# Kernel optimization log

Measured on AMD Instinct MI355X. Metric: run time of the kernel, lower is better.

## Reference

```python
import jax, jax.numpy as jnp
import numpy as np

N_NODES = 100000
N_EDGES = 1600000
IN_C, HID_C, OUT_C = 128, 128, 64


def setup_inputs() -> dict:
    key = jax.random.key(0)
    ks = jax.random.split(key, 8)
    x = jax.random.normal(ks[0], (N_NODES, IN_C), dtype=jnp.float32)
    edge_index = jax.random.randint(ks[1], (2, N_EDGES), 0, N_NODES, dtype=jnp.int64)
    # SAGEConv params: lin_l (aggregated neighbors, with bias), lin_r (root, no bias)
    s1 = 1.0 / np.sqrt(IN_C)
    s2 = 1.0 / np.sqrt(HID_C)
    W1_l = jax.random.uniform(ks[2], (IN_C, HID_C), jnp.float32, -s1, s1)
    b1_l = jnp.zeros((HID_C,), jnp.float32)
    W1_r = jax.random.uniform(ks[3], (IN_C, HID_C), jnp.float32, -s1, s1)
    W2_l = jax.random.uniform(ks[4], (HID_C, OUT_C), jnp.float32, -s2, s2)
    b2_l = jnp.zeros((OUT_C,), jnp.float32)
    W2_r = jax.random.uniform(ks[5], (HID_C, OUT_C), jnp.float32, -s2, s2)
    return {"x": x, "edge_index": edge_index, "W1_l": W1_l, "b1_l": b1_l,
            "W1_r": W1_r, "W2_l": W2_l, "b2_l": b2_l, "W2_r": W2_r}


def _sage_conv(x, src, dst, W_l, b_l, W_r):
    # gather source features, scatter-max reduce onto destinations
    msg = x[src]                                             # [E, C]
    aggr = jax.ops.segment_max(msg, dst, num_segments=N_NODES)
    aggr = jnp.where(jnp.isfinite(aggr), aggr, 0.0)          # isolated nodes -> 0 (PyG behavior)
    return aggr @ W_l + b_l + x @ W_r


def reference(x, edge_index, W1_l, b1_l, W1_r, W2_l, b2_l, W2_r):
    src, dst = edge_index[0], edge_index[1]
    h = _sage_conv(x, src, dst, W1_l, b1_l, W1_r)
    h = jax.nn.relu(h)
    # dropout is identity in eval mode
    out = _sage_conv(h, src, dst, W2_l, b2_l, W2_r)
    return out
```

## Files before the change

kernel.cpp:

```cpp
#include <hip/hip_runtime.h>
#include <cstdint>

#define NNODES 100000
#define NEDGES 1600000
#define NBKT   196
#define CAP    9216
#define BIN_CHUNK 4096
#define GBIN ((NEDGES + BIN_CHUNK - 1) / BIN_CHUNK)
#define GCVT (NNODES * 16 / 256)
#define GWPK 24

typedef __attribute__((ext_vector_type(8))) __bf16 bf16x8;
typedef __attribute__((ext_vector_type(4))) float f32x4;
typedef short v2s __attribute__((ext_vector_type(2)));

__device__ __forceinline__ unsigned short f2bf_rne(float f) {
    unsigned int u = __float_as_uint(f);
    u += 0x7fffu + ((u >> 16) & 1u);
    return (unsigned short)(u >> 16);
}
__device__ __forceinline__ unsigned encdec(unsigned u) {
    return u ^ (((u & 0x80008000u) >> 15) * 0x7FFFu);
}
__device__ __forceinline__ unsigned pkmax(unsigned a, unsigned b) {
    v2s r = __builtin_elementwise_max(__builtin_bit_cast(v2s, a), __builtin_bit_cast(v2s, b));
    return __builtin_bit_cast(unsigned, r);
}
__device__ __forceinline__ uint4 pkmax4(uint4 a, uint4 b) {
    uint4 r;
    r.x = pkmax(a.x, b.x); r.y = pkmax(a.y, b.y);
    r.z = pkmax(a.z, b.z); r.w = pkmax(a.w, b.w);
    return r;
}


__global__ __launch_bounds__(256) void prep_kernel(
        const int* __restrict__ src, const int* __restrict__ dst,
        unsigned int* __restrict__ binArr, int* __restrict__ bucketFill,
        const float4* __restrict__ xin, uint4* __restrict__ xeout,
        const float* __restrict__ W1l, const float* __restrict__ W1r,
        const float* __restrict__ W2l, const float* __restrict__ W2r,
        uint4* __restrict__ Wf1, uint4* __restrict__ Wf2, int nE) {
    if (blockIdx.x >= GBIN + GCVT) {
        int t = (blockIdx.x - GBIN - GCVT) * 256 + threadIdx.x;
        unsigned short s[8];
        if (t < 4096) {
            int h = t >> 11, kt = (t >> 9) & 3, nt = (t >> 6) & 7, lane = t & 63;
            const float* W = h ? W1r : W1l;
            int k0 = kt * 32 + (lane >> 4) * 8;
            int col = nt * 16 + (lane & 15);
#pragma unroll
            for (int jj = 0; jj < 8; ++jj) s[jj] = f2bf_rne(W[(k0 + jj) * 128 + col]);
            uint4 o;
            o.x = (unsigned)s[0] | ((unsigned)s[1] << 16);
            o.y = (unsigned)s[2] | ((unsigned)s[3] << 16);
            o.z = (unsigned)s[4] | ((unsigned)s[5] << 16);
            o.w = (unsigned)s[6] | ((unsigned)s[7] << 16);
            Wf1[t] = o;
        } else {
            int u = t - 4096;
            int h = u >> 10, kt = (u >> 8) & 3, nt = (u >> 6) & 3, lane = u & 63;
            const float* W = h ? W2r : W2l;
            int k0 = kt * 32 + (lane >> 4) * 8;
            int col = nt * 16 + (lane & 15);
#pragma unroll
            for (int jj = 0; jj < 8; ++jj) s[jj] = f2bf_rne(W[(k0 + jj) * 64 + col]);
            uint4 o;
            o.x = (unsigned)s[0] | ((unsigned)s[1] << 16);
            o.y = (unsigned)s[2] | ((unsigned)s[3] << 16);
            o.z = (unsigned)s[4] | ((unsigned)s[5] << 16);
            o.w = (unsigned)s[6] | ((unsigned)s[7] << 16);
            Wf2[u] = o;
        }
        return;
    }
    if (blockIdx.x >= GBIN) {
        int t = (blockIdx.x - GBIN) * 256 + threadIdx.x;
        int s = t / (NNODES * 8);
        int rem = t - s * (NNODES * 8);
        int n = rem >> 3, j = rem & 7;
        int f = n * 32 + s * 16 + j * 2;
        float4 v0 = xin[f], v1 = xin[f + 1];
        uint4 o;
        o.x = encdec((unsigned)f2bf_rne(v0.x) | ((unsigned)f2bf_rne(v0.y) << 16));
        o.y = encdec((unsigned)f2bf_rne(v0.z) | ((unsigned)f2bf_rne(v0.w) << 16));
        o.z = encdec((unsigned)f2bf_rne(v1.x) | ((unsigned)f2bf_rne(v1.y) << 16));
        o.w = encdec((unsigned)f2bf_rne(v1.z) | ((unsigned)f2bf_rne(v1.w) << 16));
        xeout[t] = o;
        return;
    }
    __shared__ unsigned int stage[BIN_CHUNK];
    __shared__ unsigned char bof[BIN_CHUNK];
    __shared__ int cnt[256], cstart[256], cfill[256], gbase[256];
    const int tid = threadIdx.x;
    const int blockStart = blockIdx.x * BIN_CHUNK;
    const int chunkN = min(BIN_CHUNK, nE - blockStart);
    cnt[tid] = 0;
    __syncthreads();
    int myd[16], mys[16];
#pragma unroll
    for (int i = 0; i < 16; ++i) {
        int idx = i * 256 + tid;
        if (idx < chunkN) {
            myd[i] = dst[blockStart + idx];
            mys[i] = src[blockStart + idx];
            atomicAdd(&cnt[myd[i] >> 9], 1);
        }
    }
    __syncthreads();
    int v = cnt[tid];
    for (int off = 1; off < 256; off <<= 1) {
        int add = (tid >= off) ? cnt[tid - off] : 0;
        __syncthreads();
        cnt[tid] += add;
        __syncthreads();
    }
    cstart[tid] = cnt[tid] - v;
    cfill[tid] = cnt[tid] - v;
    if (tid < NBKT && v > 0) gbase[tid] = atomicAdd(&bucketFill[tid], v);
    __syncthreads();
#pragma unroll
    for (int i = 0; i < 16; ++i) {
        int idx = i * 256 + tid;
        if (idx < chunkN) {
            int b = myd[i] >> 9;
            int p = atomicAdd(&cfill[b], 1);
            stage[p] = ((unsigned)(myd[i] & 511) << 17) | (unsigned)mys[i];
            bof[p] = (unsigned char)b;
        }
    }
    __syncthreads();
#pragma unroll
    for (int i = 0; i < 16; ++i) {
        int idx = i * 256 + tid;
        if (idx < chunkN) {
            int b = bof[idx];
            int slot = gbase[b] + (idx - cstart[b]);
            if (slot < CAP) binArr[(size_t)b * CAP + slot] = stage[idx];
        }
    }
}

__global__ __launch_bounds__(512) void build_csr_kernel(
        const unsigned int* __restrict__ binArr, const int* __restrict__ bucketFill,
        unsigned int* __restrict__ sortedSrc,
        int* __restrict__ rowBeg, int* __restrict__ rowEnd) {
    __shared__ unsigned int stage[CAP];
    __shared__ int ncnt[512], nstart[512];
    const int b = blockIdx.x;
    const int t = threadIdx.x;
    const int cnt_b = min(bucketFill[b], CAP);
    ncnt[t] = 0;
    __syncthreads();
    for (int i = t; i < cnt_b; i += 512) {
        unsigned int e = binArr[(size_t)b * CAP + i];
        stage[i] = e;
        atomicAdd(&ncnt[e >> 17], 1);
    }
    __syncthreads();
    int v = ncnt[t];
    for (int off = 1; off < 512; off <<= 1) {
        int add = (t >= off) ? ncnt[t - off] : 0;
        __syncthreads();
        ncnt[t] += add;
        __syncthreads();
    }
    int start = ncnt[t] - v;
    nstart[t] = start;
    int n = (b << 9) + t;
    if (n < NNODES) {
        rowBeg[n] = b * CAP + start;
        rowEnd[n] = b * CAP + start + v;
    }
    __syncthreads();
    for (int i = t; i < cnt_b; i += 512) {
        unsigned int e = stage[i];
        int p = atomicAdd(&nstart[e >> 17], 1);
        sortedSrc[(size_t)b * CAP + p] = e & 0x1FFFFu;
    }
}

template<int BN, bool RELU, bool ENCOUT, typename OutT>
__global__ __launch_bounds__(256) void sage_fused(
        const uint4* __restrict__ xsl,
        const int* __restrict__ rowBeg,
        const int* __restrict__ rowEnd,
        const unsigned int* __restrict__ sortedSrc,
        const uint4* __restrict__ Wf,
        const float* __restrict__ bias,
        OutT* __restrict__ C,
        int nN) {
    constexpr int NT = BN / 16;
    constexpr int NTW = BN / 64;
    __shared__ uint4 lds[16][17];
    const int wv   = threadIdx.x >> 6;
    const int lane = threadIdx.x & 63;
    const int n0   = blockIdx.x * 16;

    {
        const int s  = wv & 1;
        const int nh = wv >> 1;
        const int k  = lane >> 3;
        const int j  = lane & 7;
        const int kb = k << 3;
        const int n  = n0 + nh * 8 + k;
        const size_t srow = (size_t)s * nN;

        const int beg = rowBeg[n], end = rowEnd[n];
        const int m = end - beg;

        int maxm = m;
        maxm = max(maxm, __shfl_xor(maxm, 8));
        maxm = max(maxm, __shfl_xor(maxm, 16));
        maxm = max(maxm, __shfl_xor(maxm, 32));

        int idv0 = 0, idv1 = 0;
        if (m > 0) {
            idv0 = (int)sortedSrc[min(beg + j,     end - 1)];
            idv1 = (int)sortedSrc[min(beg + 8 + j, end - 1)];
        }
        int a0 = __shfl(idv0, kb | 0), a1 = __shfl(idv0, kb | 1);
        int a2 = __shfl(idv0, kb | 2), a3 = __shfl(idv0, kb | 3);
        int a4 = __shfl(idv0, kb | 4), a5 = __shfl(idv0, kb | 5);
        int a6 = __shfl(idv0, kb | 6), a7 = __shfl(idv0, kb | 7);
        int b0 = __shfl(idv1, kb | 0), b1 = __shfl(idv1, kb | 1);
        int b2 = __shfl(idv1, kb | 2), b3 = __shfl(idv1, kb | 3);
        int b4 = __shfl(idv1, kb | 4), b5 = __shfl(idv1, kb | 5);
        int b6 = __shfl(idv1, kb | 6), b7 = __shfl(idv1, kb | 7);
        uint4 q0  = xsl[(srow + a0) * 8 + j];
        uint4 q1  = xsl[(srow + a1) * 8 + j];
        uint4 q2  = xsl[(srow + a2) * 8 + j];
        uint4 q3  = xsl[(srow + a3) * 8 + j];
        uint4 q4  = xsl[(srow + a4) * 8 + j];
        uint4 q5  = xsl[(srow + a5) * 8 + j];
        uint4 q6  = xsl[(srow + a6) * 8 + j];
        uint4 q7  = xsl[(srow + a7) * 8 + j];
        uint4 q8  = xsl[(srow + b0) * 8 + j];
        uint4 q9  = xsl[(srow + b1) * 8 + j];
        uint4 q10 = xsl[(srow + b2) * 8 + j];
        uint4 q11 = xsl[(srow + b3) * 8 + j];
        uint4 q12 = xsl[(srow + b4) * 8 + j];
        uint4 q13 = xsl[(srow + b5) * 8 + j];
        uint4 q14 = xsl[(srow + b6) * 8 + j];
        uint4 q15 = xsl[(srow + b7) * 8 + j];
        uint4 accA = pkmax4(pkmax4(pkmax4(q0, q1), pkmax4(q2, q3)),
                            pkmax4(pkmax4(q4, q5), pkmax4(q6, q7)));
        uint4 accB = pkmax4(pkmax4(pkmax4(q8, q9), pkmax4(q10, q11)),
                            pkmax4(pkmax4(q12, q13), pkmax4(q14, q15)));
        uint4 acc = pkmax4(accA, accB);

        for (int e0 = 16; e0 < maxm; e0 += 8) {
            if (e0 < m) {
                int idt = (int)sortedSrc[min(beg + e0 + j, end - 1)];
                int t0 = __shfl(idt, kb | 0), t1 = __shfl(idt, kb | 1);
                int t2 = __shfl(idt, kb | 2), t3 = __shfl(idt, kb | 3);
                int t4 = __shfl(idt, kb | 4), t5 = __shfl(idt, kb | 5);
                int t6 = __shfl(idt, kb | 6), t7 = __shfl(idt, kb | 7);
                uint4 u0 = xsl[(srow + t0) * 8 + j];
                uint4 u1 = xsl[(srow + t1) * 8 + j];
                uint4 u2 = xsl[(srow + t2) * 8 + j];
                uint4 u3 = xsl[(srow + t3) * 8 + j];
                uint4 u4 = xsl[(srow + t4) * 8 + j];
                uint4 u5 = xsl[(srow + t5) * 8 + j];
                uint4 u6 = xsl[(srow + t6) * 8 + j];
                uint4 u7 = xsl[(srow + t7) * 8 + j];
                acc = pkmax4(acc, pkmax4(pkmax4(pkmax4(u0, u1), pkmax4(u2, u3)),
                                         pkmax4(pkmax4(u4, u5), pkmax4(u6, u7))));
            }
        }

        uint4 o;
        if (m > 0) { o = acc; }
        else       { o.x = o.y = o.z = o.w = 0u; }
        lds[nh * 8 + k][s * 8 + j] = o;
    }
    __syncthreads();

    const int quad = lane >> 4;
    const int mrow = lane & 15;
    const int r    = n0 + mrow;

    f32x4 acc[NTW];
#pragma unroll
    for (int t = 0; t < NTW; ++t) acc[t] = (f32x4){0.f, 0.f, 0.f, 0.f};

#pragma unroll
    for (int kt = 0; kt < 4; ++kt) {
        const int q = kt * 4 + quad;
        uint4 ta = lds[mrow][q];
        uint4 tr = xsl[((size_t)(q >> 3) * nN + r) * 8 + (q & 7)];
        ta.x = encdec(ta.x); ta.y = encdec(ta.y); ta.z = encdec(ta.z); ta.w = encdec(ta.w);
        tr.x = encdec(tr.x); tr.y = encdec(tr.y); tr.z = encdec(tr.z); tr.w = encdec(tr.w);
        bf16x8 aa = __builtin_bit_cast(bf16x8, ta);
        bf16x8 ar = __builtin_bit_cast(bf16x8, tr);
#pragma unroll
        for (int t = 0; t < NTW; ++t) {
            const int ct = wv * NTW + t;
            bf16x8 wb0 = __builtin_bit_cast(bf16x8, Wf[(kt * NT + ct) * 64 + lane]);
            acc[t] = __builtin_amdgcn_mfma_f32_16x16x32_bf16(aa, wb0, acc[t], 0, 0, 0);
            bf16x8 wb1 = __builtin_bit_cast(bf16x8, Wf[((4 + kt) * NT + ct) * 64 + lane]);
            acc[t] = __builtin_amdgcn_mfma_f32_16x16x32_bf16(ar, wb1, acc[t], 0, 0, 0);
        }
    }

#pragma unroll
    for (int t = 0; t < NTW; ++t) {
        const int col = (wv * NTW + t) * 16 + mrow;
        const float bv = bias[col];
#pragma unroll
        for (int rr = 0; rr < 4; ++rr) {
            const int grow = n0 + quad * 4 + rr;
            float v = acc[t][rr] + bv;
            if (RELU) v = fmaxf(v, 0.0f);
            if constexpr (ENCOUT) {
                unsigned u = f2bf_rne(v);
                u ^= ((u >> 15) & 1u) * 0x7FFFu;
                C[((size_t)(col >> 6) * nN + grow) * 64 + (col & 63)] = (OutT)u;
            } else {
                C[(size_t)grow * BN + col] = (OutT)v;
            }
        }
    }
}

extern "C" void kernel_launch(void* const* d_in, const int* in_sizes, int n_in,
                              void* d_out, int out_size, void* d_ws, size_t ws_size,
                              hipStream_t stream) {
    const float* x   = (const float*)d_in[0];
    const int*   ei  = (const int*)d_in[1];
    const float* W1l = (const float*)d_in[2];
    const float* b1l = (const float*)d_in[3];
    const float* W1r = (const float*)d_in[4];
    const float* W2l = (const float*)d_in[5];
    const float* b2l = (const float*)d_in[6];
    const float* W2r = (const float*)d_in[7];
    float* out = (float*)d_out;

    const int* src = ei;
    const int* dst = ei + NEDGES;

    char* ws = (char*)d_ws;
    unsigned short* xe    = (unsigned short*)ws; ws += (size_t)NNODES * 128 * 2;
    unsigned short* he    = (unsigned short*)ws; ws += (size_t)NNODES * 128 * 2;
    unsigned int* binArr    = (unsigned int*)ws; ws += (size_t)NBKT * CAP * 4;
    unsigned int* sortedSrc = (unsigned int*)ws; ws += (size_t)NBKT * CAP * 4;
    int* rowBeg     = (int*)ws; ws += (size_t)NNODES * 4;
    int* rowEnd     = (int*)ws; ws += (size_t)NNODES * 4;
    int* bucketFill = (int*)ws; ws += 256 * 4;
    uint4* Wf1 = (uint4*)ws; ws += 4096 * 16;
    uint4* Wf2 = (uint4*)ws; ws += 2048 * 16;

    const int gFus = NNODES / 16;

    hipMemsetAsync(bucketFill, 0, 256 * sizeof(int), stream);
    prep_kernel<<<GBIN + GCVT + GWPK, 256, 0, stream>>>(
        src, dst, binArr, bucketFill, (const float4*)x, (uint4*)xe,
        W1l, W1r, W2l, W2r, Wf1, Wf2, NEDGES);
    build_csr_kernel<<<NBKT, 512, 0, stream>>>(binArr, bucketFill, sortedSrc, rowBeg, rowEnd);

    sage_fused<128, true, true, unsigned short><<<gFus, 256, 0, stream>>>(
        (const uint4*)xe, rowBeg, rowEnd, sortedSrc, Wf1, b1l, he, NNODES);
    sage_fused<64, false, false, float><<<gFus, 256, 0, stream>>>(
        (const uint4*)he, rowBeg, rowEnd, sortedSrc, Wf2, b2l, out, NNODES);
}
```

Measured before the change: 261.0 us.

## Process two node tiles per block, overlapping second gather with first GEMM

Each block now handles 32 nodes as two 16-node tiles with double-buffered shared memory. The second tile's first 16-neighbour gather is issued before the first tile's MFMA GEMM, so gather memory latency can hide behind matrix math. Grid size is halved. The cost is higher register pressure and fewer blocks, which may lower occupancy.

```diff
diff --git a/kernel.cpp b/kernel.cpp
--- a/kernel.cpp
+++ b/kernel.cpp
@@ -181,7 +181,7 @@
 }
 
 template<int BN, bool RELU, bool ENCOUT, typename OutT>
-__global__ __launch_bounds__(256) void sage_fused(
+__global__ __launch_bounds__(256) void sage_fused2(
         const uint4* __restrict__ xsl,
         const int* __restrict__ rowBeg,
         const int* __restrict__ rowEnd,
@@ -192,135 +192,176 @@
         int nN) {
     constexpr int NT = BN / 16;
     constexpr int NTW = BN / 64;
-    __shared__ uint4 lds[16][17];
+    __shared__ uint4 ldsb[2][16][17];
     const int wv   = threadIdx.x >> 6;
     const int lane = threadIdx.x & 63;
-    const int n0   = blockIdx.x * 16;
-
-    {
-        const int s  = wv & 1;
-        const int nh = wv >> 1;
-        const int k  = lane >> 3;
-        const int j  = lane & 7;
-        const int kb = k << 3;
-        const int n  = n0 + nh * 8 + k;
-        const size_t srow = (size_t)s * nN;
-
-        const int beg = rowBeg[n], end = rowEnd[n];
-        const int m = end - beg;
-
-        int maxm = m;
-        maxm = max(maxm, __shfl_xor(maxm, 8));
-        maxm = max(maxm, __shfl_xor(maxm, 16));
-        maxm = max(maxm, __shfl_xor(maxm, 32));
-
-        int idv0 = 0, idv1 = 0;
-        if (m > 0) {
-            idv0 = (int)sortedSrc[min(beg + j,     end - 1)];
-            idv1 = (int)sortedSrc[min(beg + 8 + j, end - 1)];
-        }
-        int a0 = __shfl(idv0, kb | 0), a1 = __shfl(idv0, kb | 1);
-        int a2 = __shfl(idv0, kb | 2), a3 = __shfl(idv0, kb | 3);
-        int a4 = __shfl(idv0, kb | 4), a5 = __shfl(idv0, kb | 5);
-        int a6 = __shfl(idv0, kb | 6), a7 = __shfl(idv0, kb | 7);
-        int b0 = __shfl(idv1, kb | 0), b1 = __shfl(idv1, kb | 1);
-        int b2 = __shfl(idv1, kb | 2), b3 = __shfl(idv1, kb | 3);
-        int b4 = __shfl(idv1, kb | 4), b5 = __shfl(idv1, kb | 5);
-        int b6 = __shfl(idv1, kb | 6), b7 = __shfl(idv1, kb | 7);
-        uint4 q0  = xsl[(srow + a0) * 8 + j];
-        uint4 q1  = xsl[(srow + a1) * 8 + j];
-        uint4 q2  = xsl[(srow + a2) * 8 + j];
-        uint4 q3  = xsl[(srow + a3) * 8 + j];
-        uint4 q4  = xsl[(srow + a4) * 8 + j];
-        uint4 q5  = xsl[(srow + a5) * 8 + j];
-        uint4 q6  = xsl[(srow + a6) * 8 + j];
-        uint4 q7  = xsl[(srow + a7) * 8 + j];
-        uint4 q8  = xsl[(srow + b0) * 8 + j];
-        uint4 q9  = xsl[(srow + b1) * 8 + j];
-        uint4 q10 = xsl[(srow + b2) * 8 + j];
-        uint4 q11 = xsl[(srow + b3) * 8 + j];
-        uint4 q12 = xsl[(srow + b4) * 8 + j];
-        uint4 q13 = xsl[(srow + b5) * 8 + j];
-        uint4 q14 = xsl[(srow + b6) * 8 + j];
-        uint4 q15 = xsl[(srow + b7) * 8 + j];
-        uint4 accA = pkmax4(pkmax4(pkmax4(q0, q1), pkmax4(q2, q3)),
-                            pkmax4(pkmax4(q4, q5), pkmax4(q6, q7)));
-        uint4 accB = pkmax4(pkmax4(pkmax4(q8, q9), pkmax4(q10, q11)),
-                            pkmax4(pkmax4(q12, q13), pkmax4(q14, q15)));
-        uint4 acc = pkmax4(accA, accB);
-
-        for (int e0 = 16; e0 < maxm; e0 += 8) {
-            if (e0 < m) {
-                int idt = (int)sortedSrc[min(beg + e0 + j, end - 1)];
-                int t0 = __shfl(idt, kb | 0), t1 = __shfl(idt, kb | 1);
-                int t2 = __shfl(idt, kb | 2), t3 = __shfl(idt, kb | 3);
-                int t4 = __shfl(idt, kb | 4), t5 = __shfl(idt, kb | 5);
-                int t6 = __shfl(idt, kb | 6), t7 = __shfl(idt, kb | 7);
-                uint4 u0 = xsl[(srow + t0) * 8 + j];
-                uint4 u1 = xsl[(srow + t1) * 8 + j];
-                uint4 u2 = xsl[(srow + t2) * 8 + j];
-                uint4 u3 = xsl[(srow + t3) * 8 + j];
-                uint4 u4 = xsl[(srow + t4) * 8 + j];
-                uint4 u5 = xsl[(srow + t5) * 8 + j];
-                uint4 u6 = xsl[(srow + t6) * 8 + j];
-                uint4 u7 = xsl[(srow + t7) * 8 + j];
-                acc = pkmax4(acc, pkmax4(pkmax4(pkmax4(u0, u1), pkmax4(u2, u3)),
-                                         pkmax4(pkmax4(u4, u5), pkmax4(u6, u7))));
-            }
-        }
-
-        uint4 o;
-        if (m > 0) { o = acc; }
-        else       { o.x = o.y = o.z = o.w = 0u; }
-        lds[nh * 8 + k][s * 8 + j] = o;
-    }
-    __syncthreads();
+    const int n0   = blockIdx.x * 32;
+
+    const int s  = wv & 1;
+    const int nh = wv >> 1;
+    const int k  = lane >> 3;
+    const int j  = lane & 7;
+    const int kb = k << 3;
+    const size_t srow = (size_t)s * nN;
+    const int nloc = nh * 8 + k;
 
     const int quad = lane >> 4;
     const int mrow = lane & 15;
-    const int r    = n0 + mrow;
-
-    f32x4 acc[NTW];
-#pragma unroll
-    for (int t = 0; t < NTW; ++t) acc[t] = (f32x4){0.f, 0.f, 0.f, 0.f};
-
-#pragma unroll
-    for (int kt = 0; kt < 4; ++kt) {
-        const int q = kt * 4 + quad;
-        uint4 ta = lds[mrow][q];
-        uint4 tr = xsl[((size_t)(q >> 3) * nN + r) * 8 + (q & 7)];
-        ta.x = encdec(ta.x); ta.y = encdec(ta.y); ta.z = encdec(ta.z); ta.w = encdec(ta.w);
-        tr.x = encdec(tr.x); tr.y = encdec(tr.y); tr.z = encdec(tr.z); tr.w = encdec(tr.w);
-        bf16x8 aa = __builtin_bit_cast(bf16x8, ta);
-        bf16x8 ar = __builtin_bit_cast(bf16x8, tr);
-#pragma unroll
-        for (int t = 0; t < NTW; ++t) {
-            const int ct = wv * NTW + t;
-            bf16x8 wb0 = __builtin_bit_cast(bf16x8, Wf[(kt * NT + ct) * 64 + lane]);
-            acc[t] = __builtin_amdgcn_mfma_f32_16x16x32_bf16(aa, wb0, acc[t], 0, 0, 0);
-            bf16x8 wb1 = __builtin_bit_cast(bf16x8, Wf[((4 + kt) * NT + ct) * 64 + lane]);
-            acc[t] = __builtin_amdgcn_mfma_f32_16x16x32_bf16(ar, wb1, acc[t], 0, 0, 0);
-        }
-    }
-
-#pragma unroll
-    for (int t = 0; t < NTW; ++t) {
-        const int col = (wv * NTW + t) * 16 + mrow;
-        const float bv = bias[col];
-#pragma unroll
-        for (int rr = 0; rr < 4; ++rr) {
-            const int grow = n0 + quad * 4 + rr;
-            float v = acc[t][rr] + bv;
-            if (RELU) v = fmaxf(v, 0.0f);
-            if constexpr (ENCOUT) {
-                unsigned u = f2bf_rne(v);
-                u ^= ((u >> 15) & 1u) * 0x7FFFu;
-                C[((size_t)(col >> 6) * nN + grow) * 64 + (col & 63)] = (OutT)u;
-            } else {
-                C[(size_t)grow * BN + col] = (OutT)v;
-            }
-        }
-    }
+
+    const int nT0 = n0 + nloc, nT1 = n0 + 16 + nloc;
+    const int beg0 = rowBeg[nT0], end0 = rowEnd[nT0];
+    const int beg1 = rowBeg[nT1], end1 = rowEnd[nT1];
+    const int m0 = end0 - beg0, m1 = end1 - beg1;
+    int p0a = 0, p0b = 0, p1a = 0, p1b = 0;
+    if (m0 > 0) {
+        p0a = (int)sortedSrc[min(beg0 + j,     end0 - 1)];
+        p0b = (int)sortedSrc[min(beg0 + 8 + j, end0 - 1)];
+    }
+    if (m1 > 0) {
+        p1a = (int)sortedSrc[min(beg1 + j,     end1 - 1)];
+        p1b = (int)sortedSrc[min(beg1 + 8 + j, end1 - 1)];
+    }
+
+#define GATHER16(idvA, idvB, accOut)                                           \
+    {                                                                          \
+        int a0 = __shfl(idvA, kb | 0), a1 = __shfl(idvA, kb | 1);              \
+        int a2 = __shfl(idvA, kb | 2), a3 = __shfl(idvA, kb | 3);              \
+        int a4 = __shfl(idvA, kb | 4), a5 = __shfl(idvA, kb | 5);              \
+        int a6 = __shfl(idvA, kb | 6), a7 = __shfl(idvA, kb | 7);              \
+        int b0 = __shfl(idvB, kb | 0), b1 = __shfl(idvB, kb | 1);              \
+        int b2 = __shfl(idvB, kb | 2), b3 = __shfl(idvB, kb | 3);              \
+        int b4 = __shfl(idvB, kb | 4), b5 = __shfl(idvB, kb | 5);              \
+        int b6 = __shfl(idvB, kb | 6), b7 = __shfl(idvB, kb | 7);              \
+        uint4 q0  = xsl[(srow + a0) * 8 + j];                                  \
+        uint4 q1  = xsl[(srow + a1) * 8 + j];                                  \
+        uint4 q2  = xsl[(srow + a2) * 8 + j];                                  \
+        uint4 q3  = xsl[(srow + a3) * 8 + j];                                  \
+        uint4 q4  = xsl[(srow + a4) * 8 + j];                                  \
+        uint4 q5  = xsl[(srow + a5) * 8 + j];                                  \
+        uint4 q6  = xsl[(srow + a6) * 8 + j];                                  \
+        uint4 q7  = xsl[(srow + a7) * 8 + j];                                  \
+        uint4 q8  = xsl[(srow + b0) * 8 + j];                                  \
+        uint4 q9  = xsl[(srow + b1) * 8 + j];                                  \
+        uint4 q10 = xsl[(srow + b2) * 8 + j];                                  \
+        uint4 q11 = xsl[(srow + b3) * 8 + j];                                  \
+        uint4 q12 = xsl[(srow + b4) * 8 + j];                                  \
+        uint4 q13 = xsl[(srow + b5) * 8 + j];                                  \
+        uint4 q14 = xsl[(srow + b6) * 8 + j];                                  \
+        uint4 q15 = xsl[(srow + b7) * 8 + j];                                  \
+        accOut = pkmax4(                                                       \
+            pkmax4(pkmax4(pkmax4(q0, q1), pkmax4(q2, q3)),                     \
+                   pkmax4(pkmax4(q4, q5), pkmax4(q6, q7))),                    \
+            pkmax4(pkmax4(pkmax4(q8, q9), pkmax4(q10, q11)),                   \
+                   pkmax4(pkmax4(q12, q13), pkmax4(q14, q15))));               \
+    }
+
+#define GATHER_TAIL(beg, end, m, acc)                                          \
+    {                                                                          \
+        int maxm = m;                                                          \
+        maxm = max(maxm, __shfl_xor(maxm, 8));                                 \
+        maxm = max(maxm, __shfl_xor(maxm, 16));                                \
+        maxm = max(maxm, __shfl_xor(maxm, 32));                                \
+        for (int e0 = 16; e0 < maxm; e0 += 8) {                                \
+            if (e0 < m) {                                                      \
+                int idt = (int)sortedSrc[min(beg + e0 + j, end - 1)];          \
+                int t0 = __shfl(idt, kb | 0), t1 = __shfl(idt, kb | 1);        \
+                int t2 = __shfl(idt, kb | 2), t3 = __shfl(idt, kb | 3);        \
+                int t4 = __shfl(idt, kb | 4), t5 = __shfl(idt, kb | 5);        \
+                int t6 = __shfl(idt, kb | 6), t7 = __shfl(idt, kb | 7);        \
+                uint4 u0 = xsl[(srow + t0) * 8 + j];                           \
+                uint4 u1 = xsl[(srow + t1) * 8 + j];                           \
+                uint4 u2 = xsl[(srow + t2) * 8 + j];                           \
+                uint4 u3 = xsl[(srow + t3) * 8 + j];                           \
+                uint4 u4 = xsl[(srow + t4) * 8 + j];                           \
+                uint4 u5 = xsl[(srow + t5) * 8 + j];                           \
+                uint4 u6 = xsl[(srow + t6) * 8 + j];                           \
+                uint4 u7 = xsl[(srow + t7) * 8 + j];                           \
+                acc = pkmax4(acc,                                              \
+                    pkmax4(pkmax4(pkmax4(u0, u1), pkmax4(u2, u3)),             \
+                           pkmax4(pkmax4(u4, u5), pkmax4(u6, u7))));           \
+            }                                                                  \
+        }                                                                      \
+    }
+
+#define GEMM_TILE(tb, nb)                                                      \
+    {                                                                          \
+        f32x4 acc[NTW];                                                        \
+        _Pragma("unroll")                                                      \
+        for (int t = 0; t < NTW; ++t) acc[t] = (f32x4){0.f, 0.f, 0.f, 0.f};    \
+        const int r = (nb) + mrow;                                             \
+        _Pragma("unroll")                                                      \
+        for (int kt = 0; kt < 4; ++kt) {                                       \
+            const int q = kt * 4 + quad;                                       \
+            uint4 ta = ldsb[tb][mrow][q];                                      \
+            uint4 tr = xsl[((size_t)(q >> 3) * nN + r) * 8 + (q & 7)];         \
+            ta.x = encdec(ta.x); ta.y = encdec(ta.y);                          \
+            ta.z = encdec(ta.z); ta.w = encdec(ta.w);                          \
+            tr.x = encdec(tr.x); tr.y = encdec(tr.y);                          \
+            tr.z = encdec(tr.z); tr.w = encdec(tr.w);                          \
+            bf16x8 aa = __builtin_bit_cast(bf16x8, ta);                        \
+            bf16x8 ar = __builtin_bit_cast(bf16x8, tr);                        \
+            _Pragma("unroll")                                                  \
+            for (int t = 0; t < NTW; ++t) {                                    \
+                const int ct = wv * NTW + t;                                   \
+                bf16x8 wb0 = __builtin_bit_cast(bf16x8,                        \
+                    Wf[(kt * NT + ct) * 64 + lane]);                           \
+                acc[t] = __builtin_amdgcn_mfma_f32_16x16x32_bf16(              \
+                    aa, wb0, acc[t], 0, 0, 0);                                 \
+                bf16x8 wb1 = __builtin_bit_cast(bf16x8,                        \
+                    Wf[((4 + kt) * NT + ct) * 64 + lane]);                     \
+                acc[t] = __builtin_amdgcn_mfma_f32_16x16x32_bf16(              \
+                    ar, wb1, acc[t], 0, 0, 0);                                 \
+            }                                                                  \
+        }                                                                      \
+        _Pragma("unroll")                                                      \
+        for (int t = 0; t < NTW; ++t) {                                        \
+            const int col = (wv * NTW + t) * 16 + mrow;                        \
+            const float bv = bias[col];                                        \
+            _Pragma("unroll")                                                  \
+            for (int rr = 0; rr < 4; ++rr) {                                   \
+                const int grow = (nb) + quad * 4 + rr;                         \
+                float v = acc[t][rr] + bv;                                     \
+                if (RELU) v = fmaxf(v, 0.0f);                                  \
+                if constexpr (ENCOUT) {                                        \
+                    unsigned u = f2bf_rne(v);                                  \
+                    u ^= ((u >> 15) & 1u) * 0x7FFFu;                           \
+                    C[((size_t)(col >> 6) * nN + grow) * 64 + (col & 63)]      \
+                        = (OutT)u;                                             \
+                } else {                                                       \
+                    C[(size_t)grow * BN + col] = (OutT)v;                      \
+                }                                                              \
+            }                                                                  \
+        }                                                                      \
+    }
+
+    {
+        uint4 acc0;
+        GATHER16(p0a, p0b, acc0);
+        GATHER_TAIL(beg0, end0, m0, acc0);
+        uint4 o;
+        if (m0 > 0) { o = acc0; }
+        else        { o.x = o.y = o.z = o.w = 0u; }
+        ldsb[0][nloc][s * 8 + j] = o;
+    }
+    __syncthreads();
+
+    uint4 acc1;
+    GATHER16(p1a, p1b, acc1);
+    GEMM_TILE(0, n0);
+    GATHER_TAIL(beg1, end1, m1, acc1);
+    {
+        uint4 o;
+        if (m1 > 0) { o = acc1; }
+        else        { o.x = o.y = o.z = o.w = 0u; }
+        ldsb[1][nloc][s * 8 + j] = o;
+    }
+    __syncthreads();
+
+    GEMM_TILE(1, n0 + 16);
+
+#undef GATHER16
+#undef GATHER_TAIL
+#undef GEMM_TILE
 }
 
 extern "C" void kernel_launch(void* const* d_in, const int* in_sizes, int n_in,
@@ -350,7 +391,7 @@
     uint4* Wf1 = (uint4*)ws; ws += 4096 * 16;
     uint4* Wf2 = (uint4*)ws; ws += 2048 * 16;
 
-    const int gFus = NNODES / 16;
+    const int gFus = NNODES / 32;
 
     hipMemsetAsync(bucketFill, 0, 256 * sizeof(int), stream);
     prep_kernel<<<GBIN + GCVT + GWPK, 256, 0, stream>>>(
@@ -358,8 +399,8 @@
         W1l, W1r, W2l, W2r, Wf1, Wf2, NEDGES);
     build_csr_kernel<<<NBKT, 512, 0, stream>>>(binArr, bucketFill, sortedSrc, rowBeg, rowEnd);
 
-    sage_fused<128, true, true, unsigned short><<<gFus, 256, 0, stream>>>(
+    sage_fused2<128, true, true, unsigned short><<<gFus, 256, 0, stream>>>(
         (const uint4*)xe, rowBeg, rowEnd, sortedSrc, Wf1, b1l, he, NNODES);
-    sage_fused<64, false, false, float><<<gFus, 256, 0, stream>>>(
+    sage_fused2<64, false, false, float><<<gFus, 256, 0, stream>>>(
         (const uint4*)he, rowBeg, rowEnd, sortedSrc, Wf2, b2l, out, NNODES);
 }
```

After: 267.6 us. 1.03x slower.

## Replace bucketed CSR build with degree-count, block scan, and direct scatter

Applied to the files above, without the earlier changes.

Drops the two-level bucket binning (shared-memory staging and a per-bucket CSR kernel) and builds the CSR in three passes. Per-node global atomics count in-degrees and record each edge's rank. A per-block scan with an atomic cursor assigns row offsets, and a scatter kernel places source ids directly. This removes the fixed-capacity bucket arrays and the possible truncation at CAP, but adds 1.6M global atomics, a 16-bit rank array, an extra launch, and rows ordered non-monotonically across blocks.

```diff
diff --git a/kernel.cpp b/kernel.cpp
--- a/kernel.cpp
+++ b/kernel.cpp
@@ -3,12 +3,10 @@
 
 #define NNODES 100000
 #define NEDGES 1600000
-#define NBKT   196
-#define CAP    9216
-#define BIN_CHUNK 4096
-#define GBIN ((NEDGES + BIN_CHUNK - 1) / BIN_CHUNK)
-#define GCVT (NNODES * 16 / 256)
+#define GCNT 6250
+#define GENC 6250
 #define GWPK 24
+#define GSCN 391
 
 typedef __attribute__((ext_vector_type(8))) __bf16 bf16x8;
 typedef __attribute__((ext_vector_type(4))) float f32x4;
@@ -36,46 +34,19 @@
 
 __global__ __launch_bounds__(256) void prep_kernel(
         const int* __restrict__ src, const int* __restrict__ dst,
-        unsigned int* __restrict__ binArr, int* __restrict__ bucketFill,
+        int* __restrict__ degCnt, unsigned short* __restrict__ edgeOrd,
         const float4* __restrict__ xin, uint4* __restrict__ xeout,
         const float* __restrict__ W1l, const float* __restrict__ W1r,
         const float* __restrict__ W2l, const float* __restrict__ W2r,
-        uint4* __restrict__ Wf1, uint4* __restrict__ Wf2, int nE) {
-    if (blockIdx.x >= GBIN + GCVT) {
-        int t = (blockIdx.x - GBIN - GCVT) * 256 + threadIdx.x;
-        unsigned short s[8];
-        if (t < 4096) {
-            int h = t >> 11, kt = (t >> 9) & 3, nt = (t >> 6) & 7, lane = t & 63;
-            const float* W = h ? W1r : W1l;
-            int k0 = kt * 32 + (lane >> 4) * 8;
-            int col = nt * 16 + (lane & 15);
-#pragma unroll
-            for (int jj = 0; jj < 8; ++jj) s[jj] = f2bf_rne(W[(k0 + jj) * 128 + col]);
-            uint4 o;
-            o.x = (unsigned)s[0] | ((unsigned)s[1] << 16);
-            o.y = (unsigned)s[2] | ((unsigned)s[3] << 16);
-            o.z = (unsigned)s[4] | ((unsigned)s[5] << 16);
-            o.w = (unsigned)s[6] | ((unsigned)s[7] << 16);
-            Wf1[t] = o;
-        } else {
-            int u = t - 4096;
-            int h = u >> 10, kt = (u >> 8) & 3, nt = (u >> 6) & 3, lane = u & 63;
-            const float* W = h ? W2r : W2l;
-            int k0 = kt * 32 + (lane >> 4) * 8;
-            int col = nt * 16 + (lane & 15);
-#pragma unroll
-            for (int jj = 0; jj < 8; ++jj) s[jj] = f2bf_rne(W[(k0 + jj) * 64 + col]);
-            uint4 o;
-            o.x = (unsigned)s[0] | ((unsigned)s[1] << 16);
-            o.y = (unsigned)s[2] | ((unsigned)s[3] << 16);
-            o.z = (unsigned)s[4] | ((unsigned)s[5] << 16);
-            o.w = (unsigned)s[6] | ((unsigned)s[7] << 16);
-            Wf2[u] = o;
-        }
+        uint4* __restrict__ Wf1, uint4* __restrict__ Wf2) {
+    if (blockIdx.x < GCNT) {
+        int e = blockIdx.x * 256 + threadIdx.x;
+        int d = dst[e];
+        edgeOrd[e] = (unsigned short)atomicAdd(&degCnt[d], 1);
         return;
     }
-    if (blockIdx.x >= GBIN) {
-        int t = (blockIdx.x - GBIN) * 256 + threadIdx.x;
+    if (blockIdx.x < GCNT + GENC) {
+        int t = (blockIdx.x - GCNT) * 256 + threadIdx.x;
         int s = t / (NNODES * 8);
         int rem = t - s * (NNODES * 8);
         int n = rem >> 3, j = rem & 7;
@@ -89,95 +60,70 @@
         xeout[t] = o;
         return;
     }
-    __shared__ unsigned int stage[BIN_CHUNK];
-    __shared__ unsigned char bof[BIN_CHUNK];
-    __shared__ int cnt[256], cstart[256], cfill[256], gbase[256];
+    int t = (blockIdx.x - GCNT - GENC) * 256 + threadIdx.x;
+    unsigned short s[8];
+    if (t < 4096) {
+        int h = t >> 11, kt = (t >> 9) & 3, nt = (t >> 6) & 7, lane = t & 63;
+        const float* W = h ? W1r : W1l;
+        int k0 = kt * 32 + (lane >> 4) * 8;
+        int col = nt * 16 + (lane & 15);
+#pragma unroll
+        for (int jj = 0; jj < 8; ++jj) s[jj] = f2bf_rne(W[(k0 + jj) * 128 + col]);
+        uint4 o;
+        o.x = (unsigned)s[0] | ((unsigned)s[1] << 16);
+        o.y = (unsigned)s[2] | ((unsigned)s[3] << 16);
+        o.z = (unsigned)s[4] | ((unsigned)s[5] << 16);
+        o.w = (unsigned)s[6] | ((unsigned)s[7] << 16);
+        Wf1[t] = o;
+    } else {
+        int u = t - 4096;
+        int h = u >> 10, kt = (u >> 8) & 3, nt = (u >> 6) & 3, lane = u & 63;
+        const float* W = h ? W2r : W2l;
+        int k0 = kt * 32 + (lane >> 4) * 8;
+        int col = nt * 16 + (lane & 15);
+#pragma unroll
+        for (int jj = 0; jj < 8; ++jj) s[jj] = f2bf_rne(W[(k0 + jj) * 64 + col]);
+        uint4 o;
+        o.x = (unsigned)s[0] | ((unsigned)s[1] << 16);
+        o.y = (unsigned)s[2] | ((unsigned)s[3] << 16);
+        o.z = (unsigned)s[4] | ((unsigned)s[5] << 16);
+        o.w = (unsigned)s[6] | ((unsigned)s[7] << 16);
+        Wf2[u] = o;
+    }
+}
+
+__global__ __launch_bounds__(256) void scan_kernel(
+        const int* __restrict__ degCnt, int* __restrict__ cursor,
+        int* __restrict__ rowBeg, int* __restrict__ rowEnd) {
+    __shared__ int cnt[256];
+    __shared__ int sbase;
     const int tid = threadIdx.x;
-    const int blockStart = blockIdx.x * BIN_CHUNK;
-    const int chunkN = min(BIN_CHUNK, nE - blockStart);
-    cnt[tid] = 0;
+    const int n = blockIdx.x * 256 + tid;
+    const int d = (n < NNODES) ? degCnt[n] : 0;
+    cnt[tid] = d;
     __syncthreads();
-    int myd[16], mys[16];
-#pragma unroll
-    for (int i = 0; i < 16; ++i) {
-        int idx = i * 256 + tid;
-        if (idx < chunkN) {
-            myd[i] = dst[blockStart + idx];
-            mys[i] = src[blockStart + idx];
-            atomicAdd(&cnt[myd[i] >> 9], 1);
-        }
-    }
-    __syncthreads();
-    int v = cnt[tid];
     for (int off = 1; off < 256; off <<= 1) {
         int add = (tid >= off) ? cnt[tid - off] : 0;
         __syncthreads();
         cnt[tid] += add;
         __syncthreads();
     }
-    cstart[tid] = cnt[tid] - v;
-    cfill[tid] = cnt[tid] - v;
-    if (tid < NBKT && v > 0) gbase[tid] = atomicAdd(&bucketFill[tid], v);
+    int inc = cnt[tid];
+    if (tid == 255) sbase = atomicAdd(cursor, inc);
     __syncthreads();
-#pragma unroll
-    for (int i = 0; i < 16; ++i) {
-        int idx = i * 256 + tid;
-        if (idx < chunkN) {
-            int b = myd[i] >> 9;
-            int p = atomicAdd(&cfill[b], 1);
-            stage[p] = ((unsigned)(myd[i] & 511) << 17) | (unsigned)mys[i];
-            bof[p] = (unsigned char)b;
-        }
-    }
-    __syncthreads();
-#pragma unroll
-    for (int i = 0; i < 16; ++i) {
-        int idx = i * 256 + tid;
-        if (idx < chunkN) {
-            int b = bof[idx];
-            int slot = gbase[b] + (idx - cstart[b]);
-            if (slot < CAP) binArr[(size_t)b * CAP + slot] = stage[idx];
-        }
-    }
-}
-
-__global__ __launch_bounds__(512) void build_csr_kernel(
-        const unsigned int* __restrict__ binArr, const int* __restrict__ bucketFill,
-        unsigned int* __restrict__ sortedSrc,
-        int* __restrict__ rowBeg, int* __restrict__ rowEnd) {
-    __shared__ unsigned int stage[CAP];
-    __shared__ int ncnt[512], nstart[512];
-    const int b = blockIdx.x;
-    const int t = threadIdx.x;
-    const int cnt_b = min(bucketFill[b], CAP);
-    ncnt[t] = 0;
-    __syncthreads();
-    for (int i = t; i < cnt_b; i += 512) {
-        unsigned int e = binArr[(size_t)b * CAP + i];
-        stage[i] = e;
-        atomicAdd(&ncnt[e >> 17], 1);
-    }
-    __syncthreads();
-    int v = ncnt[t];
-    for (int off = 1; off < 512; off <<= 1) {
-        int add = (t >= off) ? ncnt[t - off] : 0;
-        __syncthreads();
-        ncnt[t] += add;
-        __syncthreads();
-    }
-    int start = ncnt[t] - v;
-    nstart[t] = start;
-    int n = (b << 9) + t;
     if (n < NNODES) {
-        rowBeg[n] = b * CAP + start;
-        rowEnd[n] = b * CAP + start + v;
-    }
-    __syncthreads();
-    for (int i = t; i < cnt_b; i += 512) {
-        unsigned int e = stage[i];
-        int p = atomicAdd(&nstart[e >> 17], 1);
-        sortedSrc[(size_t)b * CAP + p] = e & 0x1FFFFu;
-    }
+        rowBeg[n] = sbase + inc - d;
+        rowEnd[n] = sbase + inc;
+    }
+}
+
+__global__ __launch_bounds__(256) void scatter_kernel(
+        const int* __restrict__ src, const int* __restrict__ dst,
+        const unsigned short* __restrict__ edgeOrd, const int* __restrict__ rowBeg,
+        unsigned int* __restrict__ sortedSrc) {
+    int e = blockIdx.x * 256 + threadIdx.x;
+    int d = dst[e];
+    sortedSrc[rowBeg[d] + (int)edgeOrd[e]] = (unsigned)src[e];
 }
 
 template<int BN, bool RELU, bool ENCOUT, typename OutT>
@@ -342,21 +288,23 @@
     char* ws = (char*)d_ws;
     unsigned short* xe    = (unsigned short*)ws; ws += (size_t)NNODES * 128 * 2;
     unsigned short* he    = (unsigned short*)ws; ws += (size_t)NNODES * 128 * 2;
-    unsigned int* binArr    = (unsigned int*)ws; ws += (size_t)NBKT * CAP * 4;
-    unsigned int* sortedSrc = (unsigned int*)ws; ws += (size_t)NBKT * CAP * 4;
+    unsigned int* sortedSrc = (unsigned int*)ws; ws += (size_t)NEDGES * 4;
     int* rowBeg     = (int*)ws; ws += (size_t)NNODES * 4;
     int* rowEnd     = (int*)ws; ws += (size_t)NNODES * 4;
-    int* bucketFill = (int*)ws; ws += 256 * 4;
+    int* degCnt     = (int*)ws; ws += (size_t)(NNODES + 1) * 4;
+    int* cursor     = degCnt + NNODES;
+    unsigned short* edgeOrd = (unsigned short*)ws; ws += (size_t)NEDGES * 2;
     uint4* Wf1 = (uint4*)ws; ws += 4096 * 16;
     uint4* Wf2 = (uint4*)ws; ws += 2048 * 16;
 
     const int gFus = NNODES / 16;
 
-    hipMemsetAsync(bucketFill, 0, 256 * sizeof(int), stream);
-    prep_kernel<<<GBIN + GCVT + GWPK, 256, 0, stream>>>(
-        src, dst, binArr, bucketFill, (const float4*)x, (uint4*)xe,
-        W1l, W1r, W2l, W2r, Wf1, Wf2, NEDGES);
-    build_csr_kernel<<<NBKT, 512, 0, stream>>>(binArr, bucketFill, sortedSrc, rowBeg, rowEnd);
+    hipMemsetAsync(degCnt, 0, (size_t)(NNODES + 1) * 4, stream);
+    prep_kernel<<<GCNT + GENC + GWPK, 256, 0, stream>>>(
+        src, dst, degCnt, edgeOrd, (const float4*)x, (uint4*)xe,
+        W1l, W1r, W2l, W2r, Wf1, Wf2);
+    scan_kernel<<<GSCN, 256, 0, stream>>>(degCnt, cursor, rowBeg, rowEnd);
+    scatter_kernel<<<GCNT, 256, 0, stream>>>(src, dst, edgeOrd, rowBeg, sortedSrc);
 
     sage_fused<128, true, true, unsigned short><<<gFus, 256, 0, stream>>>(
         (const uint4*)xe, rowBeg, rowEnd, sortedSrc, Wf1, b1l, he, NNODES);
```

New measurement: 352.9 us. 1.35x slower.

## Rebalance prep kernels, reuse bin atomic offsets, process 32 nodes per SAGE block

Applied to the files above, without the earlier changes.

Moves the x-to-bf16 encoding out of the edge-binning kernel into extra blocks of the CSR-build kernel, so the conversion runs alongside the small 196-block CSR pass. The binning pass now keeps the offset returned by the first shared-memory count atomic, which removes the second atomic pass over a separate fill counter. The fused SAGE kernels go from 16 to 32 nodes per block with 512 threads, with waves split into row-tile and column groups. The goal is better load balance and fewer atomics, at the cost of larger blocks that may lower occupancy.

```diff
diff --git a/kernel.cpp b/kernel.cpp
--- a/kernel.cpp
+++ b/kernel.cpp
@@ -7,8 +7,8 @@
 #define CAP    9216
 #define BIN_CHUNK 4096
 #define GBIN ((NEDGES + BIN_CHUNK - 1) / BIN_CHUNK)
-#define GCVT (NNODES * 16 / 256)
 #define GWPK 24
+#define GENC (NEDGES / 512)
 
 typedef __attribute__((ext_vector_type(8))) __bf16 bf16x8;
 typedef __attribute__((ext_vector_type(4))) float f32x4;
@@ -34,15 +34,14 @@
 }
 
 
-__global__ __launch_bounds__(256) void prep_kernel(
+__global__ __launch_bounds__(256) void bin_pack_kernel(
         const int* __restrict__ src, const int* __restrict__ dst,
         unsigned int* __restrict__ binArr, int* __restrict__ bucketFill,
-        const float4* __restrict__ xin, uint4* __restrict__ xeout,
         const float* __restrict__ W1l, const float* __restrict__ W1r,
         const float* __restrict__ W2l, const float* __restrict__ W2r,
         uint4* __restrict__ Wf1, uint4* __restrict__ Wf2, int nE) {
-    if (blockIdx.x >= GBIN + GCVT) {
-        int t = (blockIdx.x - GBIN - GCVT) * 256 + threadIdx.x;
+    if (blockIdx.x >= GBIN) {
+        int t = (blockIdx.x - GBIN) * 256 + threadIdx.x;
         unsigned short s[8];
         if (t < 4096) {
             int h = t >> 11, kt = (t >> 9) & 3, nt = (t >> 6) & 7, lane = t & 63;
@@ -74,8 +73,65 @@
         }
         return;
     }
-    if (blockIdx.x >= GBIN) {
-        int t = (blockIdx.x - GBIN) * 256 + threadIdx.x;
+    __shared__ unsigned int stage[BIN_CHUNK];
+    __shared__ unsigned char bof[BIN_CHUNK];
+    __shared__ int cnt[256], cstart[256], gbase[256];
+    const int tid = threadIdx.x;
+    const int blockStart = blockIdx.x * BIN_CHUNK;
+    const int chunkN = min(BIN_CHUNK, nE - blockStart);
+    cnt[tid] = 0;
+    __syncthreads();
+    int myd[16], mys[16];
+    unsigned short myo[16];
+#pragma unroll
+    for (int i = 0; i < 16; ++i) {
+        int idx = i * 256 + tid;
+        if (idx < chunkN) {
+            myd[i] = dst[blockStart + idx];
+            mys[i] = src[blockStart + idx];
+            myo[i] = (unsigned short)atomicAdd(&cnt[myd[i] >> 9], 1);
+        }
+    }
+    __syncthreads();
+    int v = cnt[tid];
+    for (int off = 1; off < 256; off <<= 1) {
+        int add = (tid >= off) ? cnt[tid - off] : 0;
+        __syncthreads();
+        cnt[tid] += add;
+        __syncthreads();
+    }
+    cstart[tid] = cnt[tid] - v;
+    if (tid < NBKT && v > 0) gbase[tid] = atomicAdd(&bucketFill[tid], v);
+    __syncthreads();
+#pragma unroll
+    for (int i = 0; i < 16; ++i) {
+        int idx = i * 256 + tid;
+        if (idx < chunkN) {
+            int b = myd[i] >> 9;
+            int p = cstart[b] + (int)myo[i];
+            stage[p] = ((unsigned)(myd[i] & 511) << 17) | (unsigned)mys[i];
+            bof[p] = (unsigned char)b;
+        }
+    }
+    __syncthreads();
+#pragma unroll
+    for (int i = 0; i < 16; ++i) {
+        int idx = i * 256 + tid;
+        if (idx < chunkN) {
+            int b = bof[idx];
+            int slot = gbase[b] + (idx - cstart[b]);
+            if (slot < CAP) binArr[(size_t)b * CAP + slot] = stage[idx];
+        }
+    }
+}
+
+__global__ __launch_bounds__(512) void csr_encode_kernel(
+        const unsigned int* __restrict__ binArr, const int* __restrict__ bucketFill,
+        unsigned int* __restrict__ sortedSrc,
+        int* __restrict__ rowBeg, int* __restrict__ rowEnd,
+        const float4* __restrict__ xin, uint4* __restrict__ xeout) {
+    if (blockIdx.x >= NBKT) {
+        int t = (blockIdx.x - NBKT) * 512 + threadIdx.x;
         int s = t / (NNODES * 8);
         int rem = t - s * (NNODES * 8);
         int n = rem >> 3, j = rem & 7;
@@ -89,62 +145,6 @@
         xeout[t] = o;
         return;
     }
-    __shared__ unsigned int stage[BIN_CHUNK];
-    __shared__ unsigned char bof[BIN_CHUNK];
-    __shared__ int cnt[256], cstart[256], cfill[256], gbase[256];
-    const int tid = threadIdx.x;
-    const int blockStart = blockIdx.x * BIN_CHUNK;
-    const int chunkN = min(BIN_CHUNK, nE - blockStart);
-    cnt[tid] = 0;
-    __syncthreads();
-    int myd[16], mys[16];
-#pragma unroll
-    for (int i = 0; i < 16; ++i) {
-        int idx = i * 256 + tid;
-        if (idx < chunkN) {
-            myd[i] = dst[blockStart + idx];
-            mys[i] = src[blockStart + idx];
-            atomicAdd(&cnt[myd[i] >> 9], 1);
-        }
-    }
-    __syncthreads();
-    int v = cnt[tid];
-    for (int off = 1; off < 256; off <<= 1) {
-        int add = (tid >= off) ? cnt[tid - off] : 0;
-        __syncthreads();
-        cnt[tid] += add;
-        __syncthreads();
-    }
-    cstart[tid] = cnt[tid] - v;
-    cfill[tid] = cnt[tid] - v;
-    if (tid < NBKT && v > 0) gbase[tid] = atomicAdd(&bucketFill[tid], v);
-    __syncthreads();
-#pragma unroll
-    for (int i = 0; i < 16; ++i) {
-        int idx = i * 256 + tid;
-        if (idx < chunkN) {
-            int b = myd[i] >> 9;
-            int p = atomicAdd(&cfill[b], 1);
-            stage[p] = ((unsigned)(myd[i] & 511) << 17) | (unsigned)mys[i];
-            bof[p] = (unsigned char)b;
-        }
-    }
-    __syncthreads();
-#pragma unroll
-    for (int i = 0; i < 16; ++i) {
-        int idx = i * 256 + tid;
-        if (idx < chunkN) {
-            int b = bof[idx];
-            int slot = gbase[b] + (idx - cstart[b]);
-            if (slot < CAP) binArr[(size_t)b * CAP + slot] = stage[idx];
-        }
-    }
-}
-
-__global__ __launch_bounds__(512) void build_csr_kernel(
-        const unsigned int* __restrict__ binArr, const int* __restrict__ bucketFill,
-        unsigned int* __restrict__ sortedSrc,
-        int* __restrict__ rowBeg, int* __restrict__ rowEnd) {
     __shared__ unsigned int stage[CAP];
     __shared__ int ncnt[512], nstart[512];
     const int b = blockIdx.x;
@@ -181,7 +181,7 @@
 }
 
 template<int BN, bool RELU, bool ENCOUT, typename OutT>
-__global__ __launch_bounds__(256) void sage_fused(
+__global__ __launch_bounds__(512) void sage_fused(
         const uint4* __restrict__ xsl,
         const int* __restrict__ rowBeg,
         const int* __restrict__ rowEnd,
@@ -192,10 +192,10 @@
         int nN) {
     constexpr int NT = BN / 16;
     constexpr int NTW = BN / 64;
-    __shared__ uint4 lds[16][17];
+    __shared__ uint4 lds[32][17];
     const int wv   = threadIdx.x >> 6;
     const int lane = threadIdx.x & 63;
-    const int n0   = blockIdx.x * 16;
+    const int n0   = blockIdx.x * 32;
 
     {
         const int s  = wv & 1;
@@ -276,9 +276,12 @@
     }
     __syncthreads();
 
+    const int rt   = wv >> 2;
+    const int wq   = wv & 3;
     const int quad = lane >> 4;
     const int mrow = lane & 15;
-    const int r    = n0 + mrow;
+    const int rbase = n0 + rt * 16;
+    const int r     = rbase + mrow;
 
     f32x4 acc[NTW];
 #pragma unroll
@@ -287,7 +290,7 @@
 #pragma unroll
     for (int kt = 0; kt < 4; ++kt) {
         const int q = kt * 4 + quad;
-        uint4 ta = lds[mrow][q];
+        uint4 ta = lds[rt * 16 + mrow][q];
         uint4 tr = xsl[((size_t)(q >> 3) * nN + r) * 8 + (q & 7)];
         ta.x = encdec(ta.x); ta.y = encdec(ta.y); ta.z = encdec(ta.z); ta.w = encdec(ta.w);
         tr.x = encdec(tr.x); tr.y = encdec(tr.y); tr.z = encdec(tr.z); tr.w = encdec(tr.w);
@@ -295,7 +298,7 @@
         bf16x8 ar = __builtin_bit_cast(bf16x8, tr);
 #pragma unroll
         for (int t = 0; t < NTW; ++t) {
-            const int ct = wv * NTW + t;
+            const int ct = wq * NTW + t;
             bf16x8 wb0 = __builtin_bit_cast(bf16x8, Wf[(kt * NT + ct) * 64 + lane]);
             acc[t] = __builtin_amdgcn_mfma_f32_16x16x32_bf16(aa, wb0, acc[t], 0, 0, 0);
             bf16x8 wb1 = __builtin_bit_cast(bf16x8, Wf[((4 + kt) * NT + ct) * 64 + lane]);
@@ -305,11 +308,11 @@
 
 #pragma unroll
     for (int t = 0; t < NTW; ++t) {
-        const int col = (wv * NTW + t) * 16 + mrow;
+        const int col = (wq * NTW + t) * 16 + mrow;
         const float bv = bias[col];
 #pragma unroll
         for (int rr = 0; rr < 4; ++rr) {
-            const int grow = n0 + quad * 4 + rr;
+            const int grow = rbase + quad * 4 + rr;
             float v = acc[t][rr] + bv;
             if (RELU) v = fmaxf(v, 0.0f);
             if constexpr (ENCOUT) {
@@ -350,16 +353,16 @@
     uint4* Wf1 = (uint4*)ws; ws += 4096 * 16;
     uint4* Wf2 = (uint4*)ws; ws += 2048 * 16;
 
-    const int gFus = NNODES / 16;
+    const int gFus = NNODES / 32;
 
     hipMemsetAsync(bucketFill, 0, 256 * sizeof(int), stream);
-    prep_kernel<<<GBIN + GCVT + GWPK, 256, 0, stream>>>(
-        src, dst, binArr, bucketFill, (const float4*)x, (uint4*)xe,
-        W1l, W1r, W2l, W2r, Wf1, Wf2, NEDGES);
-    build_csr_kernel<<<NBKT, 512, 0, stream>>>(binArr, bucketFill, sortedSrc, rowBeg, rowEnd);
-
-    sage_fused<128, true, true, unsigned short><<<gFus, 256, 0, stream>>>(
+    bin_pack_kernel<<<GBIN + GWPK, 256, 0, stream>>>(
+        src, dst, binArr, bucketFill, W1l, W1r, W2l, W2r, Wf1, Wf2, NEDGES);
+    csr_encode_kernel<<<NBKT + GENC, 512, 0, stream>>>(
+        binArr, bucketFill, sortedSrc, rowBeg, rowEnd, (const float4*)x, (uint4*)xe);
+
+    sage_fused<128, true, true, unsigned short><<<gFus, 512, 0, stream>>>(
         (const uint4*)xe, rowBeg, rowEnd, sortedSrc, Wf1, b1l, he, NNODES);
-    sage_fused<64, false, false, float><<<gFus, 256, 0, stream>>>(
+    sage_fused<64, false, false, float><<<gFus, 512, 0, stream>>>(
         (const uint4*)he, rowBeg, rowEnd, sortedSrc, Wf2, b2l, out, NNODES);
 }
```

Result: slower. 268.6 us (+2.9%).
